# Performance work log

Measured on AMD Instinct MI355X. Metric: run time of the kernel, lower is better.

## Reference

```python
import jax, jax.numpy as jnp
import numpy as np

WS = 7       # window size
SHIFT = 3    # shift size
NH = 6       # num heads

def layernorm(x, w, b, eps=1e-5):
    mu = jnp.mean(x, axis=-1, keepdims=True)
    var = jnp.var(x, axis=-1, keepdims=True)
    return (x - mu) * jax.lax.rsqrt(var + eps) * w + b

def setup_inputs() -> dict:
    key = jax.random.key(0)
    ks = jax.random.split(key, 8)
    B, H, W, C = 16, 56, 56, 192
    hid = 4 * C
    s = lambda k, shape, fan: jax.random.normal(k, shape, jnp.float32) * (fan ** -0.5)
    return {
        "x": jax.random.normal(ks[0], (B, H, W, C), jnp.float32),
        "ln1_w": jnp.ones((C,), jnp.float32), "ln1_b": jnp.zeros((C,), jnp.float32),
        "qkv_w": s(ks[1], (C, 3 * C), C), "qkv_b": jnp.zeros((3 * C,), jnp.float32),
        "proj_w": s(ks[2], (C, C), C), "proj_b": jnp.zeros((C,), jnp.float32),
        "ln2_w": jnp.ones((C,), jnp.float32), "ln2_b": jnp.zeros((C,), jnp.float32),
        "mlp_w1": s(ks[3], (C, hid), C), "mlp_b1": jnp.zeros((hid,), jnp.float32),
        "mlp_w2": s(ks[4], (hid, C), hid), "mlp_b2": jnp.zeros((C,), jnp.float32),
    }

def reference(x, ln1_w, ln1_b, qkv_w, qkv_b, proj_w, proj_b, ln2_w, ln2_b, mlp_w1, mlp_b1, mlp_w2, mlp_b2):
    B, H, W, C = x.shape
    hd = C // NH
    scale = hd ** -0.5
    N = WS * WS

    shortcut = x
    xn = layernorm(x, ln1_w, ln1_b)
    # cyclic shift
    xs = jnp.roll(xn, shift=(-SHIFT, -SHIFT), axis=(1, 2))
    # window partition: [B*nW, N, C]
    xw = xs.reshape(B, H // WS, WS, W // WS, WS, C)
    xw = xw.transpose(0, 1, 3, 2, 4, 5).reshape(-1, N, C)

    # window attention
    qkv = xw @ qkv_w + qkv_b                       # [Bn, N, 3C]
    qkv = qkv.reshape(-1, N, 3, NH, hd).transpose(2, 0, 3, 1, 4)  # [3, Bn, NH, N, hd]
    q, k, v = qkv[0], qkv[1], qkv[2]
    attn = jnp.einsum('bhqd,bhkd->bhqk', q, k) * scale
    attn = jax.nn.softmax(attn, axis=-1)
    o = jnp.einsum('bhqk,bhkd->bhqd', attn, v)     # [Bn, NH, N, hd]
    o = o.transpose(0, 2, 1, 3).reshape(-1, N, C)
    o = o @ proj_w + proj_b

    # window reverse
    o = o.reshape(B, H // WS, W // WS, WS, WS, C)
    o = o.transpose(0, 1, 3, 2, 4, 5).reshape(B, H, W, C)
    # reverse shift
    o = jnp.roll(o, shift=(SHIFT, SHIFT), axis=(1, 2))

    x = shortcut + o
    # MLP (exact GELU, matching torch nn.GELU default)
    h = layernorm(x, ln2_w, ln2_b)
    h = jax.nn.gelu(h @ mlp_w1 + mlp_b1, approximate=False)
    x = x + (h @ mlp_w2 + mlp_b2)
    return x
```

## Files before the change

### kernel.cpp

```cpp
#include <hip/hip_runtime.h>
#include <hip/hip_bf16.h>
#include <math.h>

typedef __attribute__((ext_vector_type(8))) short short8;
typedef __attribute__((ext_vector_type(4))) float float4v;

#define C_DIM 192
#define NHEADS 6
#define NTOK 50176

__device__ __forceinline__ float bf2f(unsigned short u){
  union { unsigned int i; float f; } x; x.i = ((unsigned int)u) << 16; return x.f;
}
__device__ __forceinline__ unsigned short f2bf(float f){
  union { float f; unsigned int i; } x; x.f = f;
  unsigned int r = x.i + 0x7fff + ((x.i >> 16) & 1);
  return (unsigned short)(r >> 16);
}

__device__ __forceinline__ void gload_lds16(const unsigned short* g, unsigned short* l){
  __builtin_amdgcn_global_load_lds((const __attribute__((address_space(1))) void*)g,
                                   (__attribute__((address_space(3))) void*)l, 16, 0, 0);
}

__device__ __forceinline__ int nat_token(int r){
  int win = r / 49, n = r - win * 49;
  int b = win >> 6, rem = win & 63;
  int hs = (rem >> 3) * 7 + n / 7;
  int ws = (rem & 7) * 7 + n % 7;
  int h = hs + 3; if (h >= 56) h -= 56;
  int w = ws + 3; if (w >= 56) w -= 56;
  return (b * 56 + h) * 56 + w;
}

__global__ void transpose_kernel(const float* __restrict__ in,
                                 unsigned short* __restrict__ out, int R, int Cc){
  int idx = blockIdx.x * 256 + threadIdx.x;
  if (idx < R * Cc){ int r = idx / Cc, c = idx - r * Cc; out[(long)c * R + r] = f2bf(in[idx]); }
}

__global__ __launch_bounds__(256) void ln1_kernel(const float* __restrict__ x,
                                                  const float* __restrict__ w,
                                                  const float* __restrict__ b,
                                                  unsigned short* __restrict__ out){
  int wave = threadIdx.x >> 6, lane = threadIdx.x & 63;
  int r = blockIdx.x * 4 + wave;
  int src = nat_token(r);
  const float* xp = x + (long)src * C_DIM;
  float v0 = xp[lane], v1 = xp[lane + 64], v2 = xp[lane + 128];
  float s = v0 + v1 + v2, s2 = v0*v0 + v1*v1 + v2*v2;
  for (int m = 32; m >= 1; m >>= 1){ s += __shfl_xor(s, m, 64); s2 += __shfl_xor(s2, m, 64); }
  float mean = s * (1.f/192.f);
  float var  = s2 * (1.f/192.f) - mean*mean;
  float rs = rsqrtf(var + 1e-5f);
  unsigned short* op = out + (long)r * C_DIM;
  op[lane]       = f2bf((v0-mean)*rs*w[lane]       + b[lane]);
  op[lane + 64]  = f2bf((v1-mean)*rs*w[lane + 64]  + b[lane + 64]);
  op[lane + 128] = f2bf((v2-mean)*rs*w[lane + 128] + b[lane + 128]);
}

__global__ __launch_bounds__(256) void ln2_kernel(const float* __restrict__ y,
                                                  const float* __restrict__ w,
                                                  const float* __restrict__ b,
                                                  unsigned short* __restrict__ out){
  int wave = threadIdx.x >> 6, lane = threadIdx.x & 63;
  int r = blockIdx.x * 4 + wave;
  const float* yp = y + (long)r * C_DIM;
  float v0 = yp[lane], v1 = yp[lane + 64], v2 = yp[lane + 128];
  float s = v0 + v1 + v2, s2 = v0*v0 + v1*v1 + v2*v2;
  for (int m = 32; m >= 1; m >>= 1){ s += __shfl_xor(s, m, 64); s2 += __shfl_xor(s2, m, 64); }
  float mean = s * (1.f/192.f);
  float var  = s2 * (1.f/192.f) - mean*mean;
  float rs = rsqrtf(var + 1e-5f);
  unsigned short* op = out + (long)r * C_DIM;
  op[lane]       = f2bf((v0-mean)*rs*w[lane]       + b[lane]);
  op[lane + 64]  = f2bf((v1-mean)*rs*w[lane + 64]  + b[lane + 64]);
  op[lane + 128] = f2bf((v2-mean)*rs*w[lane + 128] + b[lane + 128]);
}

__global__ __launch_bounds__(256) void attn_kernel(const unsigned short* __restrict__ qkv,
                                                   unsigned short* __restrict__ o){
  __shared__ unsigned short pbuf[4][64][72];
  int wave = threadIdx.x >> 6, lane = threadIdx.x & 63;
  int quad = lane >> 4, l16 = lane & 15;
  int wid = blockIdx.x * 4 + wave;
  int win = wid / NHEADS, head = wid - win * NHEADS;
  const unsigned short* qp = qkv + (long)win * 49 * 576 + head * 32;
  const unsigned short* kp = qp + 192;
  const unsigned short* vp = qp + 384;

  short8 qa[4], kb[4];
  #pragma unroll
  for (int mi = 0; mi < 4; mi++){
    int m = mi * 16 + l16; if (m > 48) m = 48;
    qa[mi] = *(const short8*)&qp[(long)m * 576 + quad * 8];
  }
  #pragma unroll
  for (int ni = 0; ni < 4; ni++){
    int n = ni * 16 + l16; if (n > 48) n = 48;
    kb[ni] = *(const short8*)&kp[(long)n * 576 + quad * 8];
  }
  float4v S[4][4];
  #pragma unroll
  for (int mi = 0; mi < 4; mi++)
    #pragma unroll
    for (int ni = 0; ni < 4; ni++) S[mi][ni] = (float4v)0.f;
  #pragma unroll
  for (int mi = 0; mi < 4; mi++)
    #pragma unroll
    for (int ni = 0; ni < 4; ni++)
      S[mi][ni] = __builtin_amdgcn_mfma_f32_16x16x32_bf16(qa[mi], kb[ni], S[mi][ni], 0, 0, 0);

  #pragma unroll
  for (int mi = 0; mi < 4; mi++){
    #pragma unroll
    for (int r = 0; r < 4; r++){
      float e[4];
      float sum = 0.f;
      #pragma unroll
      for (int ni = 0; ni < 4; ni++){
        int n = ni * 16 + l16;
        float s = S[mi][ni][r] * 0.17677669529663687f;
        s = fminf(s, 80.f);
        float ev = (n <= 48) ? __expf(s) : 0.f;
        e[ni] = ev; sum += ev;
      }
      sum += __shfl_xor(sum, 1, 64);
      sum += __shfl_xor(sum, 2, 64);
      sum += __shfl_xor(sum, 4, 64);
      sum += __shfl_xor(sum, 8, 64);
      float inv = 1.f / sum;
      int m = mi * 16 + quad * 4 + r;
      #pragma unroll
      for (int ni = 0; ni < 4; ni++)
        pbuf[wave][m][ni * 16 + l16] = f2bf(e[ni] * inv);
    }
  }
  __syncthreads();

  short8 vb[2][2];
  #pragma unroll
  for (int kk2 = 0; kk2 < 2; kk2++){
    #pragma unroll
    for (int ni = 0; ni < 2; ni++){
      union { unsigned short us[8]; short8 v8; } u;
      #pragma unroll
      for (int j = 0; j < 8; j++){
        int k = kk2 * 32 + quad * 8 + j; if (k > 48) k = 48;
        u.us[j] = vp[(long)k * 576 + ni * 16 + l16];
      }
      vb[kk2][ni] = u.v8;
    }
  }

  float4v O[4][2];
  #pragma unroll
  for (int mi = 0; mi < 4; mi++)
    #pragma unroll
    for (int ni = 0; ni < 2; ni++) O[mi][ni] = (float4v)0.f;
  #pragma unroll
  for (int kk2 = 0; kk2 < 2; kk2++){
    short8 pa[4];
    #pragma unroll
    for (int mi = 0; mi < 4; mi++)
      pa[mi] = *(const short8*)&pbuf[wave][mi * 16 + l16][kk2 * 32 + quad * 8];
    #pragma unroll
    for (int mi = 0; mi < 4; mi++)
      #pragma unroll
      for (int ni = 0; ni < 2; ni++)
        O[mi][ni] = __builtin_amdgcn_mfma_f32_16x16x32_bf16(pa[mi], vb[kk2][ni], O[mi][ni], 0, 0, 0);
  }

  #pragma unroll
  for (int mi = 0; mi < 4; mi++){
    int m0 = mi * 16 + quad * 4;
    #pragma unroll
    for (int r = 0; r < 4; r++){
      if (m0 + r <= 48){
        #pragma unroll
        for (int ni = 0; ni < 2; ni++)
          o[((long)win * 49 + m0 + r) * C_DIM + head * 32 + ni * 16 + l16] = f2bf(O[mi][ni][r]);
      }
    }
  }
}

template<int EPI>
__global__ __launch_bounds__(256) void gemm_kernel(const unsigned short* __restrict__ A,
                                                   const unsigned short* __restrict__ Bt,
                                                   const float* __restrict__ bias,
                                                   unsigned short* __restrict__ Cout,
                                                   float* __restrict__ Fout,
                                                   const float* __restrict__ Xres,
                                                   int N, int K){
  __shared__ unsigned short As[128 * 64];
  __shared__ unsigned short Bs[64 * 64];
  int tid = threadIdx.x;
  int wave = tid >> 6, lane = tid & 63, quad = lane >> 4, l16 = lane & 15;
  int wm = (wave >> 1) * 64, wn = (wave & 1) * 32;
  int lrow = lane >> 3, lg = lane & 7;
  int gcol = (lg ^ lrow) * 8;
  float4v acc[4][2];
  #pragma unroll
  for (int i = 0; i < 4; i++)
    #pragma unroll
    for (int jj = 0; jj < 2; jj++) acc[i][jj] = (float4v)0.f;

  long arow0 = (long)blockIdx.x * 128;
  long brow0 = (long)blockIdx.y * 64;
  int sw = (l16 & 7);

  for (int k0 = 0; k0 < K; k0 += 64){
    #pragma unroll
    for (int t = 0; t < 4; t++){
      int ci = wave + 4 * t;
      gload_lds16(&A[(arow0 + ci * 8 + lrow) * (long)K + k0 + gcol], &As[ci * 512]);
    }
    #pragma unroll
    for (int t = 0; t < 2; t++){
      int ci = wave + 4 * t;
      gload_lds16(&Bt[(brow0 + ci * 8 + lrow) * (long)K + k0 + gcol], &Bs[ci * 512]);
    }
    __syncthreads();
    #pragma unroll
    for (int kk8 = 0; kk8 < 8; kk8 += 4){
      short8 a[4], b[2];
      #pragma unroll
      for (int mi = 0; mi < 4; mi++)
        a[mi] = *(const short8*)&As[(wm + mi*16 + l16) * 64 + ((quad + kk8) ^ sw) * 8];
      #pragma unroll
      for (int ni = 0; ni < 2; ni++)
        b[ni] = *(const short8*)&Bs[(wn + ni*16 + l16) * 64 + ((quad + kk8) ^ sw) * 8];
      #pragma unroll
      for (int mi = 0; mi < 4; mi++)
        #pragma unroll
        for (int ni = 0; ni < 2; ni++)
          acc[mi][ni] = __builtin_amdgcn_mfma_f32_16x16x32_bf16(a[mi], b[ni], acc[mi][ni], 0, 0, 0);
    }
    __syncthreads();
  }

  #pragma unroll
  for (int mi = 0; mi < 4; mi++){
    #pragma unroll
    for (int reg = 0; reg < 4; reg++){
      long r = arow0 + wm + mi*16 + quad*4 + reg;
      #pragma unroll
      for (int ni = 0; ni < 2; ni++){
        int c = (int)(brow0 + wn + ni*16 + l16);
        float v = acc[mi][ni][reg] + bias[c];
        if (EPI == 0){
          Cout[r * N + c] = f2bf(v);
        } else if (EPI == 1){
          int t = nat_token((int)r);
          long idx = (long)t * C_DIM + c;
          Fout[idx] = Xres[idx] + v;
        } else if (EPI == 2){
          float z2 = v * (1.5957691216057308f + 0.07135481282553456f * v * v);
          z2 = fminf(z2, 30.f);
          float p = __expf(z2);
          float g = v * (p / (p + 1.f));
          Cout[r * N + c] = f2bf(g);
        } else {
          long idx = r * C_DIM + c;
          Fout[idx] = Xres[idx] + v;
        }
      }
    }
  }
}

extern "C" void kernel_launch(void* const* d_in, const int* in_sizes, int n_in,
                              void* d_out, int out_size, void* d_ws, size_t ws_size,
                              hipStream_t stream){
  const float* x      = (const float*)d_in[0];
  const float* ln1_w  = (const float*)d_in[1];
  const float* ln1_b  = (const float*)d_in[2];
  const float* qkv_w  = (const float*)d_in[3];
  const float* qkv_b  = (const float*)d_in[4];
  const float* proj_w = (const float*)d_in[5];
  const float* proj_b = (const float*)d_in[6];
  const float* ln2_w  = (const float*)d_in[7];
  const float* ln2_b  = (const float*)d_in[8];
  const float* mlp_w1 = (const float*)d_in[9];
  const float* mlp_b1 = (const float*)d_in[10];
  const float* mlp_w2 = (const float*)d_in[11];
  const float* mlp_b2 = (const float*)d_in[12];
  float* out = (float*)d_out;

  char* ws = (char*)d_ws;
  unsigned short* qkv_wt = (unsigned short*)(ws);
  unsigned short* proj_wt= (unsigned short*)(ws + 221184);
  unsigned short* w1t    = (unsigned short*)(ws + 294912);
  unsigned short* w2t    = (unsigned short*)(ws + 589824);
  unsigned short* R1     = (unsigned short*)(ws + 884736);
  unsigned short* R0     = (unsigned short*)(ws + 20152320);

  unsigned short* xw   = R1;
  unsigned short* obuf = R1;
  unsigned short* hn   = R1;
  unsigned short* qkv  = R0;
  unsigned short* hbuf = R0;

  transpose_kernel<<<(110592 + 255) / 256, 256, 0, stream>>>(qkv_w, qkv_wt, 192, 576);
  transpose_kernel<<<(36864  + 255) / 256, 256, 0, stream>>>(proj_w, proj_wt, 192, 192);
  transpose_kernel<<<(147456 + 255) / 256, 256, 0, stream>>>(mlp_w1, w1t, 192, 768);
  transpose_kernel<<<(147456 + 255) / 256, 256, 0, stream>>>(mlp_w2, w2t, 768, 192);

  ln1_kernel<<<NTOK / 4, 256, 0, stream>>>(x, ln1_w, ln1_b, xw);
  gemm_kernel<0><<<dim3(392, 9),  256, 0, stream>>>(xw, qkv_wt, qkv_b, qkv, nullptr, nullptr, 576, 192);
  attn_kernel<<<(NTOK / 49) * NHEADS / 4, 256, 0, stream>>>(qkv, obuf);
  gemm_kernel<1><<<dim3(392, 3),  256, 0, stream>>>(obuf, proj_wt, proj_b, nullptr, out, x, 192, 192);
  ln2_kernel<<<NTOK / 4, 256, 0, stream>>>(out, ln2_w, ln2_b, hn);
  gemm_kernel<2><<<dim3(392, 12), 256, 0, stream>>>(hn, w1t, mlp_b1, hbuf, nullptr, nullptr, 768, 192);
  gemm_kernel<3><<<dim3(392, 3),  256, 0, stream>>>(hbuf, w2t, mlp_b2, nullptr, out, out, 192, 768);
}
```

Baseline: 271.9 us.

## Fuse MLP fc1+GELU+fc2 into a single kernel keeping hidden tile in LDS

```diff
diff --git a/kernel.cpp b/kernel.cpp
--- a/kernel.cpp
+++ b/kernel.cpp
@@ -31,6 +31,13 @@
   int h = hs + 3; if (h >= 56) h -= 56;
   int w = ws + 3; if (w >= 56) w -= 56;
   return (b * 56 + h) * 56 + w;
+}
+
+__device__ __forceinline__ float gelu_f(float v){
+  float z2 = v * (1.5957691216057308f + 0.07135481282553456f * v * v);
+  z2 = fminf(z2, 30.f);
+  float p = __expf(z2);
+  return v * (p / (p + 1.f));
 }
 
 __global__ void transpose_kernel(const float* __restrict__ in,
@@ -251,21 +258,113 @@
         float v = acc[mi][ni][reg] + bias[c];
         if (EPI == 0){
           Cout[r * N + c] = f2bf(v);
-        } else if (EPI == 1){
+        } else {
           int t = nat_token((int)r);
           long idx = (long)t * C_DIM + c;
           Fout[idx] = Xres[idx] + v;
-        } else if (EPI == 2){
-          float z2 = v * (1.5957691216057308f + 0.07135481282553456f * v * v);
-          z2 = fminf(z2, 30.f);
-          float p = __expf(z2);
-          float g = v * (p / (p + 1.f));
-          Cout[r * N + c] = f2bf(g);
-        } else {
-          long idx = r * C_DIM + c;
-          Fout[idx] = Xres[idx] + v;
         }
       }
+    }
+  }
+}
+
+__global__ __launch_bounds__(256, 2) void fused_mlp_kernel(const unsigned short* __restrict__ hn,
+                                                           const unsigned short* __restrict__ w1t,
+                                                           const float* __restrict__ b1,
+                                                           const unsigned short* __restrict__ w2t,
+                                                           const float* __restrict__ b2,
+                                                           float* __restrict__ y){
+  __shared__ __attribute__((aligned(16))) unsigned short As[3 * 64 * 64];
+  __shared__ __attribute__((aligned(16))) unsigned short Bs[192 * 64];
+  __shared__ __attribute__((aligned(16))) unsigned short Hs[64 * 72];
+  int tid = threadIdx.x;
+  int wave = tid >> 6, lane = tid & 63, quad = lane >> 4, l16 = lane & 15;
+  int lrow = lane >> 3, lg = lane & 7;
+  int gcol = (lg ^ lrow) * 8;
+  int sw = l16 & 7;
+  int wrow0 = wave * 16;
+  long arow0 = (long)blockIdx.x * 64;
+
+  float4v acc[12];
+  #pragma unroll
+  for (int i = 0; i < 12; i++) acc[i] = (float4v)0.f;
+
+  #pragma unroll
+  for (int t = 0; t < 6; t++){
+    int i = wave + 4 * t; int gg = i >> 3, br8 = (i & 7) << 3;
+    gload_lds16(&hn[(arow0 + br8 + lrow) * C_DIM + gg * 64 + gcol], &As[gg * 4096 + br8 * 64]);
+  }
+  #pragma unroll
+  for (int t = 0; t < 6; t++){
+    int i = wave + 4 * t; int gg = i >> 3, br8 = (i & 7) << 3;
+    gload_lds16(&w1t[(br8 + lrow) * 192 + gg * 64 + gcol], &Bs[gg * 4096 + br8 * 64]);
+  }
+  __syncthreads();
+
+  #pragma unroll 1
+  for (int j = 0; j < 12; j++){
+    float4v s[4];
+    #pragma unroll
+    for (int ni = 0; ni < 4; ni++) s[ni] = (float4v)0.f;
+    #pragma unroll
+    for (int kk = 0; kk < 6; kk++){
+      int gg = kk >> 1, xb = (kk & 1) * 4;
+      short8 a = *(const short8*)&As[gg * 4096 + (wrow0 + l16) * 64 + ((xb + quad) ^ sw) * 8];
+      #pragma unroll
+      for (int ni = 0; ni < 4; ni++){
+        short8 b = *(const short8*)&Bs[gg * 4096 + (ni * 16 + l16) * 64 + ((xb + quad) ^ sw) * 8];
+        s[ni] = __builtin_amdgcn_mfma_f32_16x16x32_bf16(a, b, s[ni], 0, 0, 0);
+      }
+    }
+    #pragma unroll
+    for (int ni = 0; ni < 4; ni++){
+      float bb = b1[j * 64 + ni * 16 + l16];
+      #pragma unroll
+      for (int r = 0; r < 4; r++){
+        float g = gelu_f(s[ni][r] + bb);
+        Hs[(wrow0 + quad * 4 + r) * 72 + ni * 16 + l16] = f2bf(g);
+      }
+    }
+    __syncthreads();
+
+    #pragma unroll
+    for (int t = 0; t < 6; t++){
+      int i = wave + 4 * t; int br8 = i << 3;
+      gload_lds16(&w2t[(br8 + lrow) * 768 + j * 64 + gcol], &Bs[br8 * 64]);
+    }
+    __syncthreads();
+
+    #pragma unroll
+    for (int kk = 0; kk < 2; kk++){
+      short8 pa = *(const short8*)&Hs[(wrow0 + l16) * 72 + kk * 32 + quad * 8];
+      #pragma unroll
+      for (int ni = 0; ni < 12; ni++){
+        short8 b = *(const short8*)&Bs[(ni * 16 + l16) * 64 + ((kk * 4 + quad) ^ sw) * 8];
+        acc[ni] = __builtin_amdgcn_mfma_f32_16x16x32_bf16(pa, b, acc[ni], 0, 0, 0);
+      }
+    }
+    __syncthreads();
+
+    if (j < 11){
+      #pragma unroll
+      for (int t = 0; t < 6; t++){
+        int i = wave + 4 * t; int gg = i >> 3, br8 = (i & 7) << 3;
+        gload_lds16(&w1t[((j + 1) * 64 + br8 + lrow) * 192 + gg * 64 + gcol],
+                    &Bs[gg * 4096 + br8 * 64]);
+      }
+      __syncthreads();
+    }
+  }
+
+  #pragma unroll
+  for (int ni = 0; ni < 12; ni++){
+    int c = ni * 16 + l16;
+    float bb = b2[c];
+    #pragma unroll
+    for (int r = 0; r < 4; r++){
+      long row = arow0 + wrow0 + quad * 4 + r;
+      long idx = row * C_DIM + c;
+      y[idx] = y[idx] + acc[ni][r] + bb;
     }
   }
 }
@@ -300,7 +399,6 @@
   unsigned short* obuf = R1;
   unsigned short* hn   = R1;
   unsigned short* qkv  = R0;
-  unsigned short* hbuf = R0;
 
   transpose_kernel<<<(110592 + 255) / 256, 256, 0, stream>>>(qkv_w, qkv_wt, 192, 576);
   transpose_kernel<<<(36864  + 255) / 256, 256, 0, stream>>>(proj_w, proj_wt, 192, 192);
@@ -312,6 +410,5 @@
   attn_kernel<<<(NTOK / 49) * NHEADS / 4, 256, 0, stream>>>(qkv, obuf);
   gemm_kernel<1><<<dim3(392, 3),  256, 0, stream>>>(obuf, proj_wt, proj_b, nullptr, out, x, 192, 192);
   ln2_kernel<<<NTOK / 4, 256, 0, stream>>>(out, ln2_w, ln2_b, hn);
-  gemm_kernel<2><<<dim3(392, 12), 256, 0, stream>>>(hn, w1t, mlp_b1, hbuf, nullptr, nullptr, 768, 192);
-  gemm_kernel<3><<<dim3(392, 3),  256, 0, stream>>>(hbuf, w2t, mlp_b2, nullptr, out, out, 192, 768);
-}
+  fused_mlp_kernel<<<NTOK / 64, 256, 0, stream>>>(hn, w1t, mlp_b1, w2t, mlp_b2, out);
+}
```

Result: slower. 281.1 us (+3.4%).
